# Kernel tuning notes

Measured on AMD Instinct MI355X. Metric: run time of the kernel, lower is better.

Reference implementation:

```python
import jax, jax.numpy as jnp
import numpy as np

HIDDEN = 2048
NUM_HEADS = 16
HEAD_DIM = HIDDEN // NUM_HEADS  # 128
LAYER_IDX = 0


def setup_inputs() -> dict:
    key = jax.random.key(0)
    k1, k2, k3, k4, k5 = jax.random.split(key, 5)
    B, S = 2, 2048
    hidden_states = jax.random.normal(k1, (B, S, HIDDEN), dtype=jnp.float32)
    # causal mask, broadcastable to attn shape (B, Q, H, K)
    causal = jnp.tril(jnp.ones((S, S), dtype=jnp.bool_))  # [Q, K]
    attention_mask = causal[None, :, None, :]  # [1, Q, 1, K]
    c_attn_w = jax.random.normal(k2, (HIDDEN, HIDDEN + 2 * HEAD_DIM), dtype=jnp.float32) * 0.02
    c_attn_b = jax.random.normal(k3, (HIDDEN + 2 * HEAD_DIM,), dtype=jnp.float32) * 0.02
    c_proj_w = jax.random.normal(k4, (HIDDEN, HIDDEN), dtype=jnp.float32) * 0.02
    c_proj_b = jax.random.normal(k5, (HIDDEN,), dtype=jnp.float32) * 0.02
    return {
        "hidden_states": hidden_states,
        "attention_mask": attention_mask,
        "c_attn_w": c_attn_w,
        "c_attn_b": c_attn_b,
        "c_proj_w": c_proj_w,
        "c_proj_b": c_proj_b,
    }


def reference(hidden_states, attention_mask, c_attn_w, c_attn_b, c_proj_w, c_proj_b):
    B, S, D = hidden_states.shape
    H, hd = NUM_HEADS, HEAD_DIM
    # c_attn then split into per-head query and shared (MQA) key/value
    qkv = hidden_states @ c_attn_w + c_attn_b  # [B, S, D + 2*hd]
    query = qkv[..., :D].reshape(B, S, H, hd)  # [B, Q, H, hd]
    k = qkv[..., D:D + hd]                     # [B, K, hd] shared across heads
    v = qkv[..., D + hd:]                      # [B, K, hd]
    # fp32 input => upcast=False => unscale=1, scale = 1/sqrt(head_dim)
    scale = 1.0 / jnp.sqrt(jnp.float32(hd))
    scores = jnp.einsum('bqhd,bkd->bqhk', query, k) * scale  # [B, Q, H, K]
    mask_value = jnp.finfo(jnp.float32).min
    scores = jnp.where(attention_mask, scores, mask_value)
    attn = jax.nn.softmax(scores, axis=-1)
    attn_output = jnp.einsum('bqhk,bkd->bqhd', attn, v).reshape(B, S, D)
    attn_output = attn_output @ c_proj_w + c_proj_b
    return attn_output
```

## Files before the change

### kernel.cpp

```cpp
#include <hip/hip_runtime.h>
#include <hip/hip_bf16.h>

typedef __bf16 bf16_t;
typedef __bf16 bf16x8 __attribute__((ext_vector_type(8)));
typedef __bf16 bf16x4 __attribute__((ext_vector_type(4)));
typedef float f32x4 __attribute__((ext_vector_type(4)));

#define S_LEN 2048
#define HID   2048
#define NH    16
#define HD    128
#define QKVN  2304
#define NEG_BIG (-30000.0f)
#define RESCALE_THR 8.0f

__device__ __forceinline__ void gld_lds16(const bf16_t* g, bf16_t* l) {
  __builtin_amdgcn_global_load_lds(
      (const __attribute__((address_space(1))) void*)((const void*)g),
      (__attribute__((address_space(3))) void*)((void*)l), 16, 0, 0);
}

__global__ __launch_bounds__(256) void cvt_f32_bf16_kernel(
    const float* __restrict__ in, bf16_t* __restrict__ out, int n)
{
  int i = (blockIdx.x * 256 + threadIdx.x) * 4;
  if (i < n) {
    float4 v = *(const float4*)(in + i);
    bf16x4 o;
    o[0] = (bf16_t)v.x; o[1] = (bf16_t)v.y; o[2] = (bf16_t)v.z; o[3] = (bf16_t)v.w;
    *(bf16x4*)(out + i) = o;
  }
}

__global__ __launch_bounds__(256) void transpose_cvt_kernel(
    const float* __restrict__ in, bf16_t* __restrict__ out, int K, int N)
{
  int nc = threadIdx.x & 63;
  int kg = threadIdx.x >> 6;
  int n  = blockIdx.x * 64 + nc;
  int kb = blockIdx.y * 32 + kg * 8;
  bf16x8 v;
  #pragma unroll
  for (int i = 0; i < 8; ++i) v[i] = (bf16_t)in[(size_t)(kb + i) * N + n];
  *(bf16x8*)(out + (size_t)n * K + kb) = v;
}

__global__ __launch_bounds__(256) void vt_extract_kernel(
    const bf16_t* __restrict__ qkv, bf16_t* __restrict__ vtg)
{
  int d  = threadIdx.x & 127;
  int sg = threadIdx.x >> 7;
  int b  = blockIdx.y;
  int s8 = blockIdx.x * 2 + sg;
  bf16x8 v;
  #pragma unroll
  for (int i = 0; i < 8; ++i)
    v[i] = qkv[((size_t)(b * S_LEN + s8 * 8 + i)) * QKVN + HID + HD + d];
  *(bf16x8*)(vtg + ((size_t)(b * HD + d)) * S_LEN + s8 * 8) = v;
}

template <typename OutT>
__global__ __launch_bounds__(256) void gemm_bias_kernel(
    const bf16_t* __restrict__ A, const bf16_t* __restrict__ WT,
    const float* __restrict__ bias, OutT* __restrict__ C,
    int K, int lda, int ldc)
{
  __shared__ bf16_t Ash[128 * 64];
  __shared__ bf16_t Bsh[128 * 64];

  const int tid  = threadIdx.x;
  const int wave = tid >> 6;
  const int lane = tid & 63;
  const int quad = lane >> 4;
  const int c16  = lane & 15;
  const int wm = wave >> 1;
  const int wn = wave & 1;

  int id  = (int)(blockIdx.y * gridDim.x + blockIdx.x);
  int nwg = (int)(gridDim.x * gridDim.y);
  int swz = (nwg & 7) ? id : ((id & 7) * (nwg >> 3) + (id >> 3));
  const int n0 = (swz % (int)gridDim.x) * 128;
  const int m0 = (swz / (int)gridDim.x) * 128;

  f32x4 acc[4][4] = {};

  for (int k0 = 0; k0 < K; k0 += 64) {
    __syncthreads();
    #pragma unroll
    for (int j = 0; j < 4; ++j) {
      int cbase = wave * 256 + j * 64;
      int c = cbase + lane;
      int row = c >> 3;
      int kcl = (c ^ row) & 7;
      gld_lds16(A  + (size_t)(m0 + row) * lda + k0 + kcl * 8, Ash + cbase * 8);
      gld_lds16(WT + (size_t)(n0 + row) * K   + k0 + kcl * 8, Bsh + cbase * 8);
    }
    __syncthreads();

    #pragma unroll
    for (int kk = 0; kk < 2; ++kk) {
      bf16x8 af[4], bfr[4];
      #pragma unroll
      for (int rb = 0; rb < 4; ++rb) {
        int row = wm * 64 + rb * 16 + c16;
        int kcp = ((kk * 4 + quad) ^ row) & 7;
        af[rb] = *(const bf16x8*)(Ash + row * 64 + kcp * 8);
      }
      #pragma unroll
      for (int nt = 0; nt < 4; ++nt) {
        int row = wn * 64 + nt * 16 + c16;
        int kcp = ((kk * 4 + quad) ^ row) & 7;
        bfr[nt] = *(const bf16x8*)(Bsh + row * 64 + kcp * 8);
      }
      #pragma unroll
      for (int rb = 0; rb < 4; ++rb)
        #pragma unroll
        for (int nt = 0; nt < 4; ++nt)
          acc[rb][nt] = __builtin_amdgcn_mfma_f32_16x16x32_bf16(af[rb], bfr[nt],
                                                                acc[rb][nt], 0, 0, 0);
    }
  }

  #pragma unroll
  for (int nt = 0; nt < 4; ++nt) {
    int col = n0 + wn * 64 + nt * 16 + c16;
    float bv = bias[col];
    #pragma unroll
    for (int rb = 0; rb < 4; ++rb) {
      int rbase = m0 + wm * 64 + rb * 16 + quad * 4;
      #pragma unroll
      for (int r = 0; r < 4; ++r)
        C[(size_t)(rbase + r) * ldc + col] = (OutT)(acc[rb][nt][r] + bv);
    }
  }
}

__global__ __launch_bounds__(512, 4) void mqa_attn_kernel(
    const bf16_t* __restrict__ qkv, const bf16_t* __restrict__ vtg,
    bf16_t* __restrict__ out)
{
  __shared__ bf16_t sh[17920];
  bf16_t* Ksh  = sh;
  bf16_t* VTsh = sh + 64 * 136;

  const int tid  = threadIdx.x;
  const int wv   = tid >> 6;
  const int lane = tid & 63;
  const int quad = lane >> 4;
  const int c16  = lane & 15;
  const int h = blockIdx.y;
  const int b = blockIdx.z;
  const float qscale = 0.08838834764831845f * 1.4426950408889634f;

  const bf16_t* kbase = qkv + (size_t)b * S_LEN * QKVN + HID;
  const bf16_t* vtb   = vtg + (size_t)b * HD * S_LEN;

  const int qh = ((int)blockIdx.x + h) & 15;
  const int Q  = b ? (15 - qh) : qh;
  const int q0 = Q * 128;
  const int qrow = q0 + wv * 16 + c16;
  const int ntile = 2 * Q + 2;

  const bf16_t* qp = qkv + ((size_t)(b * S_LEN + qrow)) * QKVN + h * HD;
  bf16x8 qf[4];
  #pragma unroll
  for (int ks = 0; ks < 4; ++ks) {
    bf16x8 t = *(const bf16x8*)(qp + ks * 32 + quad * 8);
    #pragma unroll
    for (int j = 0; j < 8; ++j) t[j] = (bf16_t)((float)t[j] * qscale);
    qf[ks] = t;
  }

  float m_q = NEG_BIG, l_q = 0.0f;
  f32x4 o[8] = {};

  const int prow = wv * 16 + c16;
  bf16_t* Pbase = sh + (size_t)prow * 64;
  const int rsw = prow & 7;

  for (int kt = 0; kt < ntile; ++kt) {
    __syncthreads();
    {
      const bf16_t* kb = kbase + (size_t)kt * 64 * QKVN;
      const bf16_t* vb = vtb + kt * 64;
      #pragma unroll
      for (int i = 0; i < 2; ++i) {
        int c = tid + i * 512;
        int key = c >> 4, dc = (c & 15) * 8;
        *(bf16x8*)(&Ksh[key * 136 + dc]) =
            *(const bf16x8*)(kb + (size_t)key * QKVN + dc);
      }
      #pragma unroll
      for (int i = 0; i < 2; ++i) {
        int c = tid + i * 512;
        int d = c >> 3, kc = (c & 7) * 8;
        *(bf16x8*)(&VTsh[d * 72 + kc]) =
            *(const bf16x8*)(vb + (size_t)d * S_LEN + kc);
      }
    }
    __syncthreads();

    const bool wactive = (kt * 64) <= (q0 + wv * 16 + 15);
    f32x4 sacc[4] = {};
    if (wactive) {
      __builtin_amdgcn_s_setprio(1);
      #pragma unroll
      for (int mt = 0; mt < 4; ++mt) {
        #pragma unroll
        for (int ks = 0; ks < 4; ++ks) {
          bf16x8 kf = *(const bf16x8*)(&Ksh[(mt * 16 + c16) * 136 + ks * 32 + quad * 8]);
          sacc[mt] = __builtin_amdgcn_mfma_f32_16x16x32_bf16(kf, qf[ks], sacc[mt], 0, 0, 0);
        }
      }
      __builtin_amdgcn_s_setprio(0);

      float mx = NEG_BIG;
      if (kt * 64 + 63 > q0 + wv * 16) {
        #pragma unroll
        for (int mt = 0; mt < 4; ++mt) {
          #pragma unroll
          for (int r = 0; r < 4; ++r) {
            int key = kt * 64 + mt * 16 + quad * 4 + r;
            float v = sacc[mt][r];
            if (key > qrow) v = NEG_BIG;
            sacc[mt][r] = v;
            mx = fmaxf(mx, v);
          }
        }
      } else {
        #pragma unroll
        for (int mt = 0; mt < 4; ++mt) {
          #pragma unroll
          for (int r = 0; r < 4; ++r) mx = fmaxf(mx, sacc[mt][r]);
        }
      }
      mx = fmaxf(mx, __shfl_xor(mx, 16));
      mx = fmaxf(mx, __shfl_xor(mx, 32));

      if (__any(mx > m_q + RESCALE_THR)) {
        float mn = fmaxf(m_q, mx);
        float alpha = __builtin_exp2f(m_q - mn);
        m_q = mn;
        l_q *= alpha;
        #pragma unroll
        for (int mt8 = 0; mt8 < 8; ++mt8) {
          #pragma unroll
          for (int r = 0; r < 4; ++r) o[mt8][r] *= alpha;
        }
      }

      float rs = 0.f;
      #pragma unroll
      for (int mt = 0; mt < 4; ++mt) {
        #pragma unroll
        for (int r = 0; r < 4; ++r) {
          float pe = __builtin_exp2f(sacc[mt][r] - m_q);
          sacc[mt][r] = pe;
          rs += pe;
        }
      }
      rs += __shfl_xor(rs, 16);
      rs += __shfl_xor(rs, 32);
      l_q += rs;
    }

    __syncthreads();
    if (wactive) {
      #pragma unroll
      for (int mt = 0; mt < 4; ++mt) {
        bf16x4 pk;
        #pragma unroll
        for (int r = 0; r < 4; ++r) pk[r] = (bf16_t)sacc[mt][r];
        int ch = 2 * mt + (quad >> 1);
        *(bf16x4*)(Pbase + (((ch ^ rsw) << 3) + (quad & 1) * 4)) = pk;
      }
      bf16x8 pf[2];
      #pragma unroll
      for (int kh = 0; kh < 2; ++kh) {
        int ch = 4 * kh + quad;
        pf[kh] = *(const bf16x8*)(Pbase + ((ch ^ rsw) << 3));
      }
      __builtin_amdgcn_s_setprio(1);
      #pragma unroll
      for (int mt8 = 0; mt8 < 8; ++mt8) {
        #pragma unroll
        for (int kh = 0; kh < 2; ++kh) {
          bf16x8 vf = *(const bf16x8*)(&VTsh[(mt8 * 16 + c16) * 72 + kh * 32 + quad * 8]);
          o[mt8] = __builtin_amdgcn_mfma_f32_16x16x32_bf16(vf, pf[kh], o[mt8], 0, 0, 0);
        }
      }
      __builtin_amdgcn_s_setprio(0);
    }
  }

  __syncthreads();
  float inv = 1.0f / fmaxf(l_q, 1e-20f);
  bf16_t* Osh = sh;
  #pragma unroll
  for (int mt8 = 0; mt8 < 8; ++mt8) {
    bf16x4 pk;
    #pragma unroll
    for (int r = 0; r < 4; ++r) pk[r] = (bf16_t)(o[mt8][r] * inv);
    *(bf16x4*)(&Osh[(size_t)prow * 136 + mt8 * 16 + quad * 4]) = pk;
  }
  int ql = lane >> 2, dc = lane & 3;
  #pragma unroll
  for (int i = 0; i < 4; ++i) {
    bf16x8 v = *(const bf16x8*)(&Osh[(size_t)(wv * 16 + ql) * 136 + dc * 8 + i * 32]);
    *(bf16x8*)(out + ((size_t)(b * S_LEN + q0 + wv * 16 + ql)) * HID
                   + h * HD + dc * 8 + i * 32) = v;
  }
}

extern "C" void kernel_launch(void* const* d_in, const int* in_sizes, int n_in,
                              void* d_out, int out_size, void* d_ws, size_t ws_size,
                              hipStream_t stream) {
  const float* hidden_f   = (const float*)d_in[0];
  const float* c_attn_w_f = (const float*)d_in[2];
  const float* c_attn_b_f = (const float*)d_in[3];
  const float* c_proj_w_f = (const float*)d_in[4];
  const float* c_proj_b_f = (const float*)d_in[5];
  float* out = (float*)d_out;

  const int M = 2 * S_LEN;
  const int nH  = M * HID;
  const int nWq = HID * QKVN;
  const int nWp = HID * HID;

  bf16_t* hbf   = (bf16_t*)d_ws;
  bf16_t* wqT   = hbf  + nH;
  bf16_t* wpT   = wqT  + nWq;
  bf16_t* qkv   = wpT  + nWp;
  bf16_t* attn  = qkv  + (size_t)M * QKVN;
  bf16_t* vtg   = attn + (size_t)M * HID;

  cvt_f32_bf16_kernel<<<nH / 1024, 256, 0, stream>>>(hidden_f, hbf, nH);
  dim3 gt1(QKVN / 64, HID / 32);
  transpose_cvt_kernel<<<gt1, 256, 0, stream>>>(c_attn_w_f, wqT, HID, QKVN);
  dim3 gt2(HID / 64, HID / 32);
  transpose_cvt_kernel<<<gt2, 256, 0, stream>>>(c_proj_w_f, wpT, HID, HID);

  dim3 g1(QKVN / 128, M / 128);
  gemm_bias_kernel<bf16_t><<<g1, 256, 0, stream>>>(hbf, wqT, c_attn_b_f, qkv,
                                                   HID, HID, QKVN);

  dim3 gv(S_LEN / 16, 2);
  vt_extract_kernel<<<gv, 256, 0, stream>>>(qkv, vtg);

  dim3 g2(16, NH, 2);
  mqa_attn_kernel<<<g2, 512, 0, stream>>>(qkv, vtg, attn);

  dim3 g3(HID / 128, M / 128);
  gemm_bias_kernel<float><<<g3, 256, 0, stream>>>(attn, wpT, c_proj_b_f, out,
                                                  HID, HID, HID);
}
```

Before: 333.6 us.

## Double-buffer K/V tiles with async global-to-LDS loads and XOR swizzle

The attention kernel now stages each K and V^T tile with global_load_lds into two ping-pong LDS buffers, prefetching tile kt+1 while tile kt is computed. Padded layouts are replaced by XOR-swizzled layouts to avoid bank conflicts, and P gets its own LDS region so the barrier between softmax and the PV MFMA is dropped. The aim is to hide global load latency and cut barriers per tile. In exchange LDS per block grows from about 35 KB to 80 KB, which likely lowers the number of resident 512-thread blocks per CU.

```diff
diff --git a/kernel.cpp b/kernel.cpp
--- a/kernel.cpp
+++ b/kernel.cpp
@@ -139,9 +139,7 @@
     const bf16_t* __restrict__ qkv, const bf16_t* __restrict__ vtg,
     bf16_t* __restrict__ out)
 {
-  __shared__ bf16_t sh[17920];
-  bf16_t* Ksh  = sh;
-  bf16_t* VTsh = sh + 64 * 136;
+  __shared__ bf16_t sh[40960];
 
   const int tid  = threadIdx.x;
   const int wv   = tid >> 6;
@@ -175,40 +173,48 @@
   f32x4 o[8] = {};
 
   const int prow = wv * 16 + c16;
-  bf16_t* Pbase = sh + (size_t)prow * 64;
-  const int rsw = prow & 7;
+  const int rsw  = prow & 7;
+  bf16_t* Pbase = sh + 32768 + (size_t)prow * 64;
+
+  #define STAGE(bufi, kti) do {                                              \
+    const bf16_t* kb_ = kbase + (size_t)(kti) * 64 * QKVN;                   \
+    const bf16_t* vb_ = vtb + (kti) * 64;                                    \
+    bf16_t* Kd_ = sh + (bufi) * 8192;                                        \
+    bf16_t* Vd_ = sh + 16384 + (bufi) * 8192;                                \
+    _Pragma("unroll")                                                        \
+    for (int i_ = 0; i_ < 2; ++i_) {                                         \
+      int c_ = tid + i_ * 512;                                               \
+      int r_ = c_ >> 4, lc_ = (c_ & 15) ^ (r_ & 7);                          \
+      gld_lds16(kb_ + (size_t)r_ * QKVN + lc_ * 8, Kd_ + (c_ & ~63) * 8);    \
+    }                                                                        \
+    _Pragma("unroll")                                                        \
+    for (int i_ = 0; i_ < 2; ++i_) {                                         \
+      int c_ = tid + i_ * 512;                                               \
+      int r_ = c_ >> 3, lc_ = (c_ & 7) ^ (r_ & 7);                           \
+      gld_lds16(vb_ + (size_t)r_ * S_LEN + lc_ * 8, Vd_ + (c_ & ~63) * 8);   \
+    }                                                                        \
+  } while (0)
+
+  STAGE(0, 0);
+  int cur = 0;
 
   for (int kt = 0; kt < ntile; ++kt) {
     __syncthreads();
-    {
-      const bf16_t* kb = kbase + (size_t)kt * 64 * QKVN;
-      const bf16_t* vb = vtb + kt * 64;
-      #pragma unroll
-      for (int i = 0; i < 2; ++i) {
-        int c = tid + i * 512;
-        int key = c >> 4, dc = (c & 15) * 8;
-        *(bf16x8*)(&Ksh[key * 136 + dc]) =
-            *(const bf16x8*)(kb + (size_t)key * QKVN + dc);
-      }
-      #pragma unroll
-      for (int i = 0; i < 2; ++i) {
-        int c = tid + i * 512;
-        int d = c >> 3, kc = (c & 7) * 8;
-        *(bf16x8*)(&VTsh[d * 72 + kc]) =
-            *(const bf16x8*)(vb + (size_t)d * S_LEN + kc);
-      }
-    }
-    __syncthreads();
-
+    if (kt + 1 < ntile) STAGE(cur ^ 1, kt + 1);
+
+    const bf16_t* Kc = sh + cur * 8192;
+    const bf16_t* Vc = sh + 16384 + cur * 8192;
     const bool wactive = (kt * 64) <= (q0 + wv * 16 + 15);
-    f32x4 sacc[4] = {};
     if (wactive) {
+      f32x4 sacc[4] = {};
       __builtin_amdgcn_s_setprio(1);
       #pragma unroll
       for (int mt = 0; mt < 4; ++mt) {
+        int krow = mt * 16 + c16;
         #pragma unroll
         for (int ks = 0; ks < 4; ++ks) {
-          bf16x8 kf = *(const bf16x8*)(&Ksh[(mt * 16 + c16) * 136 + ks * 32 + quad * 8]);
+          bf16x8 kf = *(const bf16x8*)(Kc + krow * 128 +
+                                       (((ks * 4 + quad) ^ (krow & 7)) << 3));
           sacc[mt] = __builtin_amdgcn_mfma_f32_16x16x32_bf16(kf, qf[ks], sacc[mt], 0, 0, 0);
         }
       }
@@ -262,10 +268,7 @@
       rs += __shfl_xor(rs, 16);
       rs += __shfl_xor(rs, 32);
       l_q += rs;
-    }
-
-    __syncthreads();
-    if (wactive) {
+
       #pragma unroll
       for (int mt = 0; mt < 4; ++mt) {
         bf16x4 pk;
@@ -276,22 +279,25 @@
       }
       bf16x8 pf[2];
       #pragma unroll
-      for (int kh = 0; kh < 2; ++kh) {
-        int ch = 4 * kh + quad;
-        pf[kh] = *(const bf16x8*)(Pbase + ((ch ^ rsw) << 3));
-      }
+      for (int kh = 0; kh < 2; ++kh)
+        pf[kh] = *(const bf16x8*)(Pbase + (((4 * kh + quad) ^ rsw) << 3));
+
       __builtin_amdgcn_s_setprio(1);
       #pragma unroll
       for (int mt8 = 0; mt8 < 8; ++mt8) {
+        int vrow = mt8 * 16 + c16;
         #pragma unroll
         for (int kh = 0; kh < 2; ++kh) {
-          bf16x8 vf = *(const bf16x8*)(&VTsh[(mt8 * 16 + c16) * 72 + kh * 32 + quad * 8]);
+          bf16x8 vf = *(const bf16x8*)(Vc + vrow * 64 +
+                                       (((kh * 4 + quad) ^ (vrow & 7)) << 3));
           o[mt8] = __builtin_amdgcn_mfma_f32_16x16x32_bf16(vf, pf[kh], o[mt8], 0, 0, 0);
         }
       }
       __builtin_amdgcn_s_setprio(0);
     }
-  }
+    cur ^= 1;
+  }
+  #undef STAGE
 
   __syncthreads();
   float inv = 1.0f / fmaxf(l_q, 1e-20f);
```

Result: faster. 311.0 us (-6.8%).
